# Performance work log

Measured on AMD Instinct MI355X. Metric: run time of the kernel, lower is better.

The kernel has to match this reference:

```python
import jax, jax.numpy as jnp
import numpy as np
import math

HEAD_DIM = 128
LAMBDA_INIT = 0.8


def setup_inputs() -> dict:
    key = jax.random.key(0)
    ks = jax.random.split(key, 5)
    B, H, HKV, S, D = 1, 16, 4, 2048, HEAD_DIM
    return {
        "q1": jax.random.normal(ks[0], (B, H, S, D), jnp.float32),
        "k1": jax.random.normal(ks[1], (B, HKV, S, D), jnp.float32),
        "v": jax.random.normal(ks[2], (B, HKV, S, D), jnp.float32),
        "q2": jax.random.normal(ks[3], (B, H, S, D), jnp.float32),
        "k2": jax.random.normal(ks[4], (B, HKV, S, D), jnp.float32),
        "lambda_log": jnp.full((1,), math.log(LAMBDA_INIT), jnp.float32),
    }


def _sdpa(q, k, v, scale):
    # q: [b,h,s,d]; k,v already repeated to h heads
    s = jnp.einsum("bhqd,bhkd->bhqk", q, k) * scale
    w = jax.nn.softmax(s, axis=-1)
    return jnp.einsum("bhqk,bhkd->bhqd", w, v)


def reference(q1, k1, v, q2, k2, lambda_log):
    H = q1.shape[1]
    HKV = k1.shape[1]
    rep = H // HKV
    if rep > 1:
        k1 = jnp.repeat(k1, rep, axis=1)
        k2 = jnp.repeat(k2, rep, axis=1)
        v = jnp.repeat(v, rep, axis=1)
    scale = q1.shape[-1] ** -0.5
    attn1 = _sdpa(q1, k1, v, scale)
    attn2 = _sdpa(q2, k2, v, scale)
    lam = jnp.exp(lambda_log).astype(q1.dtype)  # shape (1,), broadcasts
    return attn1 - lam * attn2
```

## Files before the change

### kernel.cpp

```cpp
#include <hip/hip_runtime.h>
#include <hip/hip_bf16.h>
#include <stdint.h>

#define D 128
#define SEQ 2048
#define NH 16
#define KVB 64
#define NTILE 32
#define BLOCK_Q 128

typedef float f32x4  __attribute__((ext_vector_type(4)));
typedef float f32x16 __attribute__((ext_vector_type(16)));
typedef short bf16x8 __attribute__((ext_vector_type(8)));

__device__ __forceinline__ unsigned cvtpk(float lo, float hi){
    unsigned r;
    asm("v_cvt_pk_bf16_f32 %0, %1, %2" : "=v"(r) : "v"(lo), "v"(hi));
    return r;
}

__global__ __launch_bounds__(256) void prep(const float* __restrict__ k1,
                                            const float* __restrict__ k2,
                                            const float* __restrict__ v,
                                            char* __restrict__ ws)
{
    int cid = blockIdx.x * 256 + threadIdx.x;
    if (cid < 262144){
        const float* src = (cid & 131072) ? k2 : k1;
        int r    = cid & 131071;
        int grow = r >> 4;
        int c16  = r & 15;
        const float* p = src + (size_t)grow * D + ((c16 ^ (grow & 7)) << 3);
        f32x4 a = *(const f32x4*)p;
        f32x4 b = *(const f32x4*)(p + 4);
        uint4 w;
        w.x = cvtpk(a[0], a[1]); w.y = cvtpk(a[2], a[3]);
        w.z = cvtpk(b[0], b[1]); w.w = cvtpk(b[2], b[3]);
        *(uint4*)(ws + (size_t)cid * 16) = w;
    } else {
        int r   = cid - 262144;
        int d   = (r >> 3) & 127;
        int c16 = r & 7;
        int gk  = ((r >> 10) << 6) + ((c16 ^ (d & 7)) << 3);
        const float* p = v + (size_t)gk * D + d;
        uint4 w;
        w.x = cvtpk(p[0*D], p[1*D]);
        w.y = cvtpk(p[2*D], p[3*D]);
        w.z = cvtpk(p[4*D], p[5*D]);
        w.w = cvtpk(p[6*D], p[7*D]);
        *(uint4*)(ws + 4194304 + (size_t)r * 16) = w;
    }
}

struct Buf { char k1[16384]; char k2[16384]; char vt[16384]; };
union LdsU { Buf buf[2]; float oepi[BLOCK_Q * D]; };

__global__ __launch_bounds__(512, 2)
void diffattn(const float* __restrict__ q1, const float* __restrict__ q2,
              const float* __restrict__ ll, const char* __restrict__ ws,
              float* __restrict__ out)
{
    __shared__ LdsU lds;
    const int tid  = threadIdx.x;
    const int lane = tid & 63;
    const int wid  = tid >> 6;
    const int atn  = wid >> 2;
    const int wq   = wid & 3;
    const int g    = lane >> 5;
    const int ql   = lane & 31;

    const int bid  = blockIdx.x;
    const int sbid = (bid & 7) * 32 + (bid >> 3);
    const int qb   = sbid & 15;
    const int h    = sbid >> 4;
    const int kvh  = h >> 2;

    auto stage = [&](int b, int t){
        const char* base = ws + ((size_t)(kvh * NTILE + t) << 14) + (lane << 4);
        char* lb = (char*)&lds.buf[b];
        #pragma unroll
        for (int j = 0; j < 6; ++j){
            int ci  = wid * 6 + j;
            int mat = ci >> 4, sub = ci & 15;
            __builtin_amdgcn_global_load_lds(
                (const __attribute__((address_space(1))) void*)(base + (size_t)mat * 2097152 + (sub << 10)),
                (__attribute__((address_space(3))) void*)(lb + mat * 16384 + (sub << 10)),
                16, 0, 0);
        }
    };
    stage(0, 0);

    const float* Qbase = (atn ? q2 : q1)
        + ((size_t)h * SEQ + (size_t)qb * BLOCK_Q + wq * 32 + ql) * D;
    const float qsc = 0.08838834764831845f * 1.4426950408889634f;
    bf16x8 qf[8];
    #pragma unroll
    for (int dc = 0; dc < 8; ++dc){
        const float* p = Qbase + dc * 16 + g * 8;
        f32x4 a = *(const f32x4*)(p);
        f32x4 b = *(const f32x4*)(p + 4);
        union { bf16x8 v; unsigned u[4]; } u;
        u.u[0] = cvtpk(a[0] * qsc, a[1] * qsc);
        u.u[1] = cvtpk(a[2] * qsc, a[3] * qsc);
        u.u[2] = cvtpk(b[0] * qsc, b[1] * qsc);
        u.u[3] = cvtpk(b[2] * qsc, b[3] * qsc);
        qf[dc] = u.v;
    }

    f32x16 ot[4];
    #pragma unroll
    for (int i = 0; i < 4; ++i){
        #pragma unroll
        for (int e = 0; e < 16; ++e) ot[i][e] = 0.f;
    }
    float mrun = -1e30f, lrun = 0.f;

    __syncthreads();

    for (int t = 0; t < NTILE; ++t){
        const int cur = t & 1;
        if (t + 1 < NTILE) stage(cur ^ 1, t + 1);

        const char* kt = atn ? lds.buf[cur].k2 : lds.buf[cur].k1;
        const char* vt = lds.buf[cur].vt;

        f32x16 st[2];
        __builtin_amdgcn_s_setprio(1);
        #pragma unroll
        for (int kb = 0; kb < 2; ++kb){
            f32x16 acc;
            #pragma unroll
            for (int e = 0; e < 16; ++e) acc[e] = 0.f;
            const int krow = kb * 32 + ql;
            const int kswz = (krow & 7) << 4;
            #pragma unroll
            for (int dc = 0; dc < 8; ++dc){
                bf16x8 kf = *(const bf16x8*)(kt + ((krow * 256 + dc * 32 + g * 16) ^ kswz));
                acc = __builtin_amdgcn_mfma_f32_32x32x16_bf16(kf, qf[dc], acc, 0, 0, 0);
            }
            st[kb] = acc;
        }
        __builtin_amdgcn_s_setprio(0);

        float tmax = -1e30f;
        #pragma unroll
        for (int kb = 0; kb < 2; ++kb){
            #pragma unroll
            for (int e = 0; e < 16; ++e) tmax = fmaxf(tmax, st[kb][e]);
        }
        tmax = fmaxf(tmax, __shfl_xor(tmax, 32));
        if (!__all(tmax <= mrun + 8.f)){
            float mnew = fmaxf(mrun, tmax);
            float corr = exp2f(mrun - mnew);
            lrun *= corr;
            #pragma unroll
            for (int i = 0; i < 4; ++i) ot[i] = ot[i] * corr;
            mrun = mnew;
        }
        float p[2][16];
        float ps = 0.f;
        #pragma unroll
        for (int kb = 0; kb < 2; ++kb){
            #pragma unroll
            for (int e = 0; e < 16; ++e){
                float pe = exp2f(st[kb][e] - mrun);
                p[kb][e] = pe; ps += pe;
            }
        }
        ps += __shfl_xor(ps, 32);
        lrun += ps;

        unsigned W[2][4][2];
        #pragma unroll
        for (int kb = 0; kb < 2; ++kb){
            #pragma unroll
            for (int hh = 0; hh < 4; ++hh){
                #pragma unroll
                for (int jj = 0; jj < 2; ++jj)
                    W[kb][hh][jj] = cvtpk(p[kb][4*hh + 2*jj], p[kb][4*hh + 2*jj + 1]);
            }
        }
        bf16x8 pb[4];
        #pragma unroll
        for (int kc = 0; kc < 4; ++kc){
            const int kb = kc >> 1, b0 = 2 * (kc & 1);
            union { bf16x8 v; unsigned u[4]; } pu;
            #pragma unroll
            for (int j = 0; j < 4; ++j){
                const int gsrc = j >> 1, jj = j & 1;
                unsigned wlo = W[kb][b0][jj];
                unsigned whi = W[kb][b0 + 1][jj];
                unsigned loc = g ? whi : wlo;
                unsigned oth = g ? wlo : whi;
                unsigned rem = (unsigned)__shfl_xor((int)oth, 32);
                pu.u[j] = (gsrc == g) ? loc : rem;
            }
            pb[kc] = pu.v;
        }

        __builtin_amdgcn_s_setprio(1);
        #pragma unroll
        for (int db = 0; db < 4; ++db){
            const int drow = db * 32 + ql;
            const int vswz = (drow & 7) << 4;
            #pragma unroll
            for (int kc = 0; kc < 4; ++kc){
                bf16x8 vf = *(const bf16x8*)(vt + ((drow * 128 + kc * 32 + g * 16) ^ vswz));
                ot[db] = __builtin_amdgcn_mfma_f32_32x32x16_bf16(vf, pb[kc], ot[db], 0, 0, 0);
            }
        }
        __builtin_amdgcn_s_setprio(0);
        __syncthreads();
    }

    const float lam = expf(ll[0]);
    const float inv = 1.f / lrun;
    const int rowl = wq * 32 + ql;
    const int eswz = (rowl & 7) << 2;

    if (atn == 1){
        const float s = -lam * inv;
        #pragma unroll
        for (int db = 0; db < 4; ++db){
            #pragma unroll
            for (int e = 0; e < 16; ++e){
                int d = db * 32 + (e & 3) + 8 * (e >> 2) + 4 * g;
                lds.oepi[rowl * 128 + (d ^ eswz)] = ot[db][e] * s;
            }
        }
    }
    __syncthreads();
    if (atn == 0){
        #pragma unroll
        for (int db = 0; db < 4; ++db){
            #pragma unroll
            for (int e = 0; e < 16; ++e){
                int d = db * 32 + (e & 3) + 8 * (e >> 2) + 4 * g;
                int idx = rowl * 128 + (d ^ eswz);
                lds.oepi[idx] = ot[db][e] * inv + lds.oepi[idx];
            }
        }
    }
    __syncthreads();

    const size_t obase = ((size_t)h * SEQ + (size_t)qb * BLOCK_Q) * D;
    const int row = tid >> 2;
    const int q4  = tid & 3;
    const int sw  = (row & 7) << 2;
    #pragma unroll
    for (int j = 0; j < 8; ++j){
        int c = q4 * 32 + j * 4;
        f32x4 val = *(const f32x4*)&lds.oepi[row * 128 + (c ^ sw)];
        *(f32x4*)(out + obase + (size_t)row * D + c) = val;
    }
}

extern "C" void kernel_launch(void* const* d_in, const int* in_sizes, int n_in,
                              void* d_out, int out_size, void* d_ws, size_t ws_size,
                              hipStream_t stream)
{
    (void)in_sizes; (void)n_in; (void)out_size; (void)ws_size;
    const float* q1 = (const float*)d_in[0];
    const float* k1 = (const float*)d_in[1];
    const float* v  = (const float*)d_in[2];
    const float* q2 = (const float*)d_in[3];
    const float* k2 = (const float*)d_in[4];
    const float* ll = (const float*)d_in[5];
    prep<<<1536, 256, 0, stream>>>(k1, k2, v, (char*)d_ws);
    diffattn<<<256, 512, 0, stream>>>(q1, q2, ll, (const char*)d_ws, (float*)d_out);
}
```

Before: 183.7 us.

## Give each wave two query sub-tiles and transpose V through LDS in prep

The attention kernel drops to 256 threads, with each wave handling 64 query rows as two 32-row sub-tiles. Each K and V fragment read from LDS now feeds two MFMAs, which halves LDS fragment traffic per FLOP, at the cost of double the accumulator registers and one block per CU. The prep kernel's V transpose now reads coalesced rows into a padded LDS buffer and writes the transposed bf16 tiles from there, replacing the old strided column gathers. This also shrinks prep's grid.

```diff
diff --git a/kernel.cpp b/kernel.cpp
--- a/kernel.cpp
+++ b/kernel.cpp
@@ -8,6 +8,7 @@
 #define KVB 64
 #define NTILE 32
 #define BLOCK_Q 128
+#define QT 64
 
 typedef float f32x4  __attribute__((ext_vector_type(4)));
 typedef float f32x16 __attribute__((ext_vector_type(16)));
@@ -19,43 +20,69 @@
     return r;
 }
 
+#define VSTRIDE 130
 __global__ __launch_bounds__(256) void prep(const float* __restrict__ k1,
                                             const float* __restrict__ k2,
                                             const float* __restrict__ v,
                                             char* __restrict__ ws)
 {
-    int cid = blockIdx.x * 256 + threadIdx.x;
-    if (cid < 262144){
+    __shared__ unsigned short vlds[64 * VSTRIDE];
+    const int b = blockIdx.x;
+    if (b < 1024){
+        int cid = b * 256 + threadIdx.x;
         const float* src = (cid & 131072) ? k2 : k1;
         int r    = cid & 131071;
         int grow = r >> 4;
         int c16  = r & 15;
         const float* p = src + (size_t)grow * D + ((c16 ^ (grow & 7)) << 3);
         f32x4 a = *(const f32x4*)p;
-        f32x4 b = *(const f32x4*)(p + 4);
+        f32x4 c = *(const f32x4*)(p + 4);
         uint4 w;
         w.x = cvtpk(a[0], a[1]); w.y = cvtpk(a[2], a[3]);
-        w.z = cvtpk(b[0], b[1]); w.w = cvtpk(b[2], b[3]);
+        w.z = cvtpk(c[0], c[1]); w.w = cvtpk(c[2], c[3]);
         *(uint4*)(ws + (size_t)cid * 16) = w;
     } else {
-        int r   = cid - 262144;
-        int d   = (r >> 3) & 127;
-        int c16 = r & 7;
-        int gk  = ((r >> 10) << 6) + ((c16 ^ (d & 7)) << 3);
-        const float* p = v + (size_t)gk * D + d;
-        uint4 w;
-        w.x = cvtpk(p[0*D], p[1*D]);
-        w.y = cvtpk(p[2*D], p[3*D]);
-        w.z = cvtpk(p[4*D], p[5*D]);
-        w.w = cvtpk(p[6*D], p[7*D]);
-        *(uint4*)(ws + 4194304 + (size_t)r * 16) = w;
+        const int vt  = b - 1024;
+        const int tid = threadIdx.x;
+        const size_t gkb = (size_t)vt * 64;
+        const int key = tid >> 2, cg = tid & 3;
+        const float* vp = v + (gkb + key) * D + cg * 32;
+        #pragma unroll
+        for (int i = 0; i < 8; ++i){
+            f32x4 x = *(const f32x4*)(vp + i * 4);
+            unsigned lo = cvtpk(x[0], x[1]);
+            unsigned hi = cvtpk(x[2], x[3]);
+            unsigned* dst = (unsigned*)&vlds[key * VSTRIDE + cg * 32 + i * 4];
+            dst[0] = lo; dst[1] = hi;
+        }
+        __syncthreads();
+        char* outb = ws + 4194304 + ((size_t)vt << 14);
+        #pragma unroll
+        for (int i = 0; i < 4; ++i){
+            int c   = tid + 256 * i;
+            int d   = c >> 3;
+            int c16 = c & 7;
+            int m   = (c16 ^ (d & 7)) << 3;
+            unsigned v0 = vlds[(m + 0) * VSTRIDE + d];
+            unsigned v1 = vlds[(m + 1) * VSTRIDE + d];
+            unsigned v2 = vlds[(m + 2) * VSTRIDE + d];
+            unsigned v3 = vlds[(m + 3) * VSTRIDE + d];
+            unsigned v4 = vlds[(m + 4) * VSTRIDE + d];
+            unsigned v5 = vlds[(m + 5) * VSTRIDE + d];
+            unsigned v6 = vlds[(m + 6) * VSTRIDE + d];
+            unsigned v7 = vlds[(m + 7) * VSTRIDE + d];
+            uint4 w;
+            w.x = v0 | (v1 << 16); w.y = v2 | (v3 << 16);
+            w.z = v4 | (v5 << 16); w.w = v6 | (v7 << 16);
+            *(uint4*)(outb + (size_t)c * 16) = w;
+        }
     }
 }
 
 struct Buf { char k1[16384]; char k2[16384]; char vt[16384]; };
 union LdsU { Buf buf[2]; float oepi[BLOCK_Q * D]; };
 
-__global__ __launch_bounds__(512, 2)
+__global__ __launch_bounds__(256, 1)
 void diffattn(const float* __restrict__ q1, const float* __restrict__ q2,
               const float* __restrict__ ll, const char* __restrict__ ws,
               float* __restrict__ out)
@@ -64,8 +91,8 @@
     const int tid  = threadIdx.x;
     const int lane = tid & 63;
     const int wid  = tid >> 6;
-    const int atn  = wid >> 2;
-    const int wq   = wid & 3;
+    const int atn  = wid >> 1;
+    const int wq   = wid & 1;
     const int g    = lane >> 5;
     const int ql   = lane & 31;
 
@@ -75,12 +102,12 @@
     const int h    = sbid >> 4;
     const int kvh  = h >> 2;
 
-    auto stage = [&](int b, int t){
+    auto stage = [&](int bsel, int t){
         const char* base = ws + ((size_t)(kvh * NTILE + t) << 14) + (lane << 4);
-        char* lb = (char*)&lds.buf[b];
-        #pragma unroll
-        for (int j = 0; j < 6; ++j){
-            int ci  = wid * 6 + j;
+        char* lb = (char*)&lds.buf[bsel];
+        #pragma unroll
+        for (int j = 0; j < 12; ++j){
+            int ci  = wid * 12 + j;
             int mat = ci >> 4, sub = ci & 15;
             __builtin_amdgcn_global_load_lds(
                 (const __attribute__((address_space(1))) void*)(base + (size_t)mat * 2097152 + (sub << 10)),
@@ -90,30 +117,34 @@
     };
     stage(0, 0);
 
-    const float* Qbase = (atn ? q2 : q1)
-        + ((size_t)h * SEQ + (size_t)qb * BLOCK_Q + wq * 32 + ql) * D;
     const float qsc = 0.08838834764831845f * 1.4426950408889634f;
-    bf16x8 qf[8];
+    bf16x8 qf[2][8];
     #pragma unroll
-    for (int dc = 0; dc < 8; ++dc){
-        const float* p = Qbase + dc * 16 + g * 8;
-        f32x4 a = *(const f32x4*)(p);
-        f32x4 b = *(const f32x4*)(p + 4);
-        union { bf16x8 v; unsigned u[4]; } u;
-        u.u[0] = cvtpk(a[0] * qsc, a[1] * qsc);
-        u.u[1] = cvtpk(a[2] * qsc, a[3] * qsc);
-        u.u[2] = cvtpk(b[0] * qsc, b[1] * qsc);
-        u.u[3] = cvtpk(b[2] * qsc, b[3] * qsc);
-        qf[dc] = u.v;
-    }
-
-    f32x16 ot[4];
+    for (int qs = 0; qs < 2; ++qs){
+        const float* Qbase = (atn ? q2 : q1)
+            + ((size_t)h * SEQ + (size_t)qb * BLOCK_Q + wq * QT + qs * 32 + ql) * D;
+        #pragma unroll
+        for (int dc = 0; dc < 8; ++dc){
+            const float* p = Qbase + dc * 16 + g * 8;
+            f32x4 a = *(const f32x4*)(p);
+            f32x4 c = *(const f32x4*)(p + 4);
+            union { bf16x8 v; unsigned u[4]; } u;
+            u.u[0] = cvtpk(a[0] * qsc, a[1] * qsc);
+            u.u[1] = cvtpk(a[2] * qsc, a[3] * qsc);
+            u.u[2] = cvtpk(c[0] * qsc, c[1] * qsc);
+            u.u[3] = cvtpk(c[2] * qsc, c[3] * qsc);
+            qf[qs][dc] = u.v;
+        }
+    }
+
+    f32x16 ot[2][4];
     #pragma unroll
-    for (int i = 0; i < 4; ++i){
-        #pragma unroll
-        for (int e = 0; e < 16; ++e) ot[i][e] = 0.f;
-    }
-    float mrun = -1e30f, lrun = 0.f;
+    for (int qs = 0; qs < 2; ++qs)
+        #pragma unroll
+        for (int i = 0; i < 4; ++i)
+            #pragma unroll
+            for (int e = 0; e < 16; ++e) ot[qs][i][e] = 0.f;
+    float mrun[2] = {-1e30f, -1e30f}, lrun[2] = {0.f, 0.f};
 
     __syncthreads();
 
@@ -124,78 +155,78 @@
         const char* kt = atn ? lds.buf[cur].k2 : lds.buf[cur].k1;
         const char* vt = lds.buf[cur].vt;
 
-        f32x16 st[2];
+        f32x16 st[2][2];
         __builtin_amdgcn_s_setprio(1);
         #pragma unroll
         for (int kb = 0; kb < 2; ++kb){
-            f32x16 acc;
-            #pragma unroll
-            for (int e = 0; e < 16; ++e) acc[e] = 0.f;
+            #pragma unroll
+            for (int qs = 0; qs < 2; ++qs)
+                #pragma unroll
+                for (int e = 0; e < 16; ++e) st[qs][kb][e] = 0.f;
             const int krow = kb * 32 + ql;
             const int kswz = (krow & 7) << 4;
             #pragma unroll
             for (int dc = 0; dc < 8; ++dc){
                 bf16x8 kf = *(const bf16x8*)(kt + ((krow * 256 + dc * 32 + g * 16) ^ kswz));
-                acc = __builtin_amdgcn_mfma_f32_32x32x16_bf16(kf, qf[dc], acc, 0, 0, 0);
+                st[0][kb] = __builtin_amdgcn_mfma_f32_32x32x16_bf16(kf, qf[0][dc], st[0][kb], 0, 0, 0);
+                st[1][kb] = __builtin_amdgcn_mfma_f32_32x32x16_bf16(kf, qf[1][dc], st[1][kb], 0, 0, 0);
             }
-            st[kb] = acc;
         }
         __builtin_amdgcn_s_setprio(0);
 
-        float tmax = -1e30f;
-        #pragma unroll
-        for (int kb = 0; kb < 2; ++kb){
-            #pragma unroll
-            for (int e = 0; e < 16; ++e) tmax = fmaxf(tmax, st[kb][e]);
-        }
-        tmax = fmaxf(tmax, __shfl_xor(tmax, 32));
-        if (!__all(tmax <= mrun + 8.f)){
-            float mnew = fmaxf(mrun, tmax);
-            float corr = exp2f(mrun - mnew);
-            lrun *= corr;
-            #pragma unroll
-            for (int i = 0; i < 4; ++i) ot[i] = ot[i] * corr;
-            mrun = mnew;
-        }
-        float p[2][16];
-        float ps = 0.f;
-        #pragma unroll
-        for (int kb = 0; kb < 2; ++kb){
-            #pragma unroll
-            for (int e = 0; e < 16; ++e){
-                float pe = exp2f(st[kb][e] - mrun);
-                p[kb][e] = pe; ps += pe;
+        bf16x8 pb[2][4];
+        #pragma unroll
+        for (int qs = 0; qs < 2; ++qs){
+            float tmax = -1e30f;
+            #pragma unroll
+            for (int kb = 0; kb < 2; ++kb)
+                #pragma unroll
+                for (int e = 0; e < 16; ++e) tmax = fmaxf(tmax, st[qs][kb][e]);
+            tmax = fmaxf(tmax, __shfl_xor(tmax, 32));
+            if (!__all(tmax <= mrun[qs] + 8.f)){
+                float mnew = fmaxf(mrun[qs], tmax);
+                float corr = exp2f(mrun[qs] - mnew);
+                lrun[qs] *= corr;
+                #pragma unroll
+                for (int i = 0; i < 4; ++i) ot[qs][i] = ot[qs][i] * corr;
+                mrun[qs] = mnew;
             }
-        }
-        ps += __shfl_xor(ps, 32);
-        lrun += ps;
-
-        unsigned W[2][4][2];
-        #pragma unroll
-        for (int kb = 0; kb < 2; ++kb){
-            #pragma unroll
-            for (int hh = 0; hh < 4; ++hh){
-                #pragma unroll
-                for (int jj = 0; jj < 2; ++jj)
-                    W[kb][hh][jj] = cvtpk(p[kb][4*hh + 2*jj], p[kb][4*hh + 2*jj + 1]);
+            float p[2][16];
+            float ps = 0.f;
+            #pragma unroll
+            for (int kb = 0; kb < 2; ++kb)
+                #pragma unroll
+                for (int e = 0; e < 16; ++e){
+                    float pe = exp2f(st[qs][kb][e] - mrun[qs]);
+                    p[kb][e] = pe; ps += pe;
+                }
+            ps += __shfl_xor(ps, 32);
+            lrun[qs] += ps;
+
+            unsigned W[2][4][2];
+            #pragma unroll
+            for (int kb = 0; kb < 2; ++kb)
+                #pragma unroll
+                for (int hh = 0; hh < 4; ++hh)
+                    #pragma unroll
+                    for (int jj = 0; jj < 2; ++jj)
+                        W[kb][hh][jj] = cvtpk(p[kb][4*hh + 2*jj], p[kb][4*hh + 2*jj + 1]);
+            #pragma unroll
+            for (int kc = 0; kc < 4; ++kc){
+                const int kb = kc >> 1, b0 = 2 * (kc & 1);
+                union { bf16x8 v; unsigned u[4]; } pu;
+                #pragma unroll
+                for (int j = 0; j < 4; ++j){
+                    const int gsrc = j >> 1, jj = j & 1;
+                    unsigned wlo = W[kb][b0][jj];
+                    unsigned whi = W[kb][b0 + 1][jj];
+                    unsigned loc = g ? whi : wlo;
+                    unsigned oth = g ? wlo : whi;
+                    unsigned rem = (unsigned)__shfl_xor((int)oth, 32);
+                    pu.u[j] = (gsrc == g) ? loc : rem;
+                }
+                pb[qs][kc] = pu.v;
             }
-        }
-        bf16x8 pb[4];
-        #pragma unroll
-        for (int kc = 0; kc < 4; ++kc){
-            const int kb = kc >> 1, b0 = 2 * (kc & 1);
-            union { bf16x8 v; unsigned u[4]; } pu;
-            #pragma unroll
-            for (int j = 0; j < 4; ++j){
-                const int gsrc = j >> 1, jj = j & 1;
-                unsigned wlo = W[kb][b0][jj];
-                unsigned whi = W[kb][b0 + 1][jj];
-                unsigned loc = g ? whi : wlo;
-                unsigned oth = g ? wlo : whi;
-                unsigned rem = (unsigned)__shfl_xor((int)oth, 32);
-                pu.u[j] = (gsrc == g) ? loc : rem;
-            }
-            pb[kc] = pu.v;
         }
 
         __builtin_amdgcn_s_setprio(1);
@@ -206,7 +237,8 @@
             #pragma unroll
             for (int kc = 0; kc < 4; ++kc){
                 bf16x8 vf = *(const bf16x8*)(vt + ((drow * 128 + kc * 32 + g * 16) ^ vswz));
-                ot[db] = __builtin_amdgcn_mfma_f32_32x32x16_bf16(vf, pb[kc], ot[db], 0, 0, 0);
+                ot[0][db] = __builtin_amdgcn_mfma_f32_32x32x16_bf16(vf, pb[0][kc], ot[0][db], 0, 0, 0);
+                ot[1][db] = __builtin_amdgcn_mfma_f32_32x32x16_bf16(vf, pb[1][kc], ot[1][db], 0, 0, 0);
             }
         }
         __builtin_amdgcn_s_setprio(0);
@@ -214,43 +246,58 @@
     }
 
     const float lam = expf(ll[0]);
-    const float inv = 1.f / lrun;
-    const int rowl = wq * 32 + ql;
-    const int eswz = (rowl & 7) << 2;
 
     if (atn == 1){
-        const float s = -lam * inv;
-        #pragma unroll
-        for (int db = 0; db < 4; ++db){
-            #pragma unroll
-            for (int e = 0; e < 16; ++e){
-                int d = db * 32 + (e & 3) + 8 * (e >> 2) + 4 * g;
-                lds.oepi[rowl * 128 + (d ^ eswz)] = ot[db][e] * s;
-            }
+        #pragma unroll
+        for (int qs = 0; qs < 2; ++qs){
+            const float s = -lam / lrun[qs];
+            const int rowl = wq * QT + qs * 32 + ql;
+            const int eswz = (rowl & 7) << 2;
+            #pragma unroll
+            for (int db = 0; db < 4; ++db)
+                #pragma unroll
+                for (int e = 0; e < 16; ++e){
+                    int d = db * 32 + (e & 3) + 8 * (e >> 2) + 4 * g;
+                    lds.oepi[rowl * 128 + (d ^ eswz)] = ot[qs][db][e] * s;
+                }
         }
     }
     __syncthreads();
     if (atn == 0){
         #pragma unroll
-        for (int db = 0; db < 4; ++db){
-            #pragma unroll
-            for (int e = 0; e < 16; ++e){
-                int d = db * 32 + (e & 3) + 8 * (e >> 2) + 4 * g;
-                int idx = rowl * 128 + (d ^ eswz);
-                lds.oepi[idx] = ot[db][e] * inv + lds.oepi[idx];
-            }
+        for (int qs = 0; qs < 2; ++qs){
+            const float inv = 1.f / lrun[qs];
+            const int rowl = wq * QT + qs * 32 + ql;
+            const int eswz = (rowl & 7) << 2;
+            #pragma unroll
+            for (int db = 0; db < 4; ++db)
+                #pragma unroll
+                for (int e = 0; e < 16; ++e){
+                    int d = db * 32 + (e & 3) + 8 * (e >> 2) + 4 * g;
+                    int idx = rowl * 128 + (d ^ eswz);
+                    lds.oepi[idx] = ot[qs][db][e] * inv + lds.oepi[idx];
+                }
         }
     }
     __syncthreads();
 
     const size_t obase = ((size_t)h * SEQ + (size_t)qb * BLOCK_Q) * D;
-    const int row = tid >> 2;
-    const int q4  = tid & 3;
+    const int row = tid >> 1;
+    const int ch  = (tid & 1) * 64;
     const int sw  = (row & 7) << 2;
     #pragma unroll
-    for (int j = 0; j < 8; ++j){
-        int c = q4 * 32 + j * 4;
+    for (int j = 0; j < 4; ++j){
+        int c = ch + j * 16;
         f32x4 val = *(const f32x4*)&lds.oepi[row * 128 + (c ^ sw)];
+        *(f32x4*)(out + obase + (size_t)row * D + c) = val;
+        c += 4;
+        val = *(const f32x4*)&lds.oepi[row * 128 + (c ^ sw)];
+        *(f32x4*)(out + obase + (size_t)row * D + c) = val;
+        c += 4;
+        val = *(const f32x4*)&lds.oepi[row * 128 + (c ^ sw)];
+        *(f32x4*)(out + obase + (size_t)row * D + c) = val;
+        c += 4;
+        val = *(const f32x4*)&lds.oepi[row * 128 + (c ^ sw)];
         *(f32x4*)(out + obase + (size_t)row * D + c) = val;
     }
 }
@@ -266,6 +313,6 @@
     const float* q2 = (const float*)d_in[3];
     const float* k2 = (const float*)d_in[4];
     const float* ll = (const float*)d_in[5];
-    prep<<<1536, 256, 0, stream>>>(k1, k2, v, (char*)d_ws);
-    diffattn<<<256, 512, 0, stream>>>(q1, q2, ll, (const char*)d_ws, (float*)d_out);
+    prep<<<1152, 256, 0, stream>>>(k1, k2, v, (char*)d_ws);
+    diffattn<<<256, 256, 0, stream>>>(q1, q2, ll, (const char*)d_ws, (float*)d_out);
 }
```

New measurement: 226.1 us. +23.1%, slower.

## Halve query and KV tiles, fold max offset into MFMA init, transpose V via LDS

Applied to the files above, without the earlier changes.

The attention kernel now uses 64-row query blocks and 32-key tiles, launched as 512 blocks of 256 threads instead of 256 blocks of 512. This halves LDS per buffer and gives more blocks to spread across CUs. The running max is pre-subtracted by initializing the QK accumulator with -m, which removes a subtract per score. The prep kernel now transposes V through shared memory with coalesced fp32 reads, replacing the old strided global reads. The trade-off is twice as many KV-tile iterations and barriers, and K/V tiles are reloaded once per smaller query block.

```diff
diff --git a/kernel.cpp b/kernel.cpp
--- a/kernel.cpp
+++ b/kernel.cpp
@@ -5,9 +5,9 @@
 #define D 128
 #define SEQ 2048
 #define NH 16
-#define KVB 64
-#define NTILE 32
-#define BLOCK_Q 128
+#define KVB 32
+#define NTILE 64
+#define BLOCK_Q 64
 
 typedef float f32x4  __attribute__((ext_vector_type(4)));
 typedef float f32x16 __attribute__((ext_vector_type(16)));
@@ -19,43 +19,71 @@
     return r;
 }
 
+#define VSTRIDE 130
 __global__ __launch_bounds__(256) void prep(const float* __restrict__ k1,
                                             const float* __restrict__ k2,
                                             const float* __restrict__ v,
                                             char* __restrict__ ws)
 {
-    int cid = blockIdx.x * 256 + threadIdx.x;
-    if (cid < 262144){
+    __shared__ unsigned short vlds[64 * VSTRIDE];
+    const int b = blockIdx.x;
+    if (b < 1024){
+        int cid = b * 256 + threadIdx.x;
         const float* src = (cid & 131072) ? k2 : k1;
         int r    = cid & 131071;
         int grow = r >> 4;
         int c16  = r & 15;
         const float* p = src + (size_t)grow * D + ((c16 ^ (grow & 7)) << 3);
         f32x4 a = *(const f32x4*)p;
-        f32x4 b = *(const f32x4*)(p + 4);
+        f32x4 c = *(const f32x4*)(p + 4);
         uint4 w;
         w.x = cvtpk(a[0], a[1]); w.y = cvtpk(a[2], a[3]);
-        w.z = cvtpk(b[0], b[1]); w.w = cvtpk(b[2], b[3]);
+        w.z = cvtpk(c[0], c[1]); w.w = cvtpk(c[2], c[3]);
         *(uint4*)(ws + (size_t)cid * 16) = w;
     } else {
-        int r   = cid - 262144;
-        int d   = (r >> 3) & 127;
-        int c16 = r & 7;
-        int gk  = ((r >> 10) << 6) + ((c16 ^ (d & 7)) << 3);
-        const float* p = v + (size_t)gk * D + d;
-        uint4 w;
-        w.x = cvtpk(p[0*D], p[1*D]);
-        w.y = cvtpk(p[2*D], p[3*D]);
-        w.z = cvtpk(p[4*D], p[5*D]);
-        w.w = cvtpk(p[6*D], p[7*D]);
-        *(uint4*)(ws + 4194304 + (size_t)r * 16) = w;
-    }
-}
-
-struct Buf { char k1[16384]; char k2[16384]; char vt[16384]; };
+        const int vt  = b - 1024;
+        const int tid = threadIdx.x;
+        const int key = tid >> 2, cg = tid & 3;
+        const float* vp = v + (size_t)(vt * 64 + key) * D + cg * 32;
+        #pragma unroll
+        for (int i = 0; i < 8; ++i){
+            f32x4 x = *(const f32x4*)(vp + i * 4);
+            unsigned lo = cvtpk(x[0], x[1]);
+            unsigned hi = cvtpk(x[2], x[3]);
+            unsigned* dst = (unsigned*)&vlds[key * VSTRIDE + cg * 32 + i * 4];
+            dst[0] = lo; dst[1] = hi;
+        }
+        __syncthreads();
+        #pragma unroll
+        for (int tt = 0; tt < 2; ++tt){
+            char* outb = ws + 4194304 + (((size_t)vt * 2 + tt) << 13);
+            #pragma unroll
+            for (int i = 0; i < 2; ++i){
+                int c = tid + 256 * i;
+                int d = c >> 2;
+                int s = c & 3;
+                int m = tt * 32 + ((s ^ (d & 3)) << 3);
+                unsigned v0 = vlds[(m + 0) * VSTRIDE + d];
+                unsigned v1 = vlds[(m + 1) * VSTRIDE + d];
+                unsigned v2 = vlds[(m + 2) * VSTRIDE + d];
+                unsigned v3 = vlds[(m + 3) * VSTRIDE + d];
+                unsigned v4 = vlds[(m + 4) * VSTRIDE + d];
+                unsigned v5 = vlds[(m + 5) * VSTRIDE + d];
+                unsigned v6 = vlds[(m + 6) * VSTRIDE + d];
+                unsigned v7 = vlds[(m + 7) * VSTRIDE + d];
+                uint4 w;
+                w.x = v0 | (v1 << 16); w.y = v2 | (v3 << 16);
+                w.z = v4 | (v5 << 16); w.w = v6 | (v7 << 16);
+                *(uint4*)(outb + (size_t)c * 16) = w;
+            }
+        }
+    }
+}
+
+struct Buf { char k1[8192]; char k2[8192]; char vt[8192]; };
 union LdsU { Buf buf[2]; float oepi[BLOCK_Q * D]; };
 
-__global__ __launch_bounds__(512, 2)
+__global__ __launch_bounds__(256, 2)
 void diffattn(const float* __restrict__ q1, const float* __restrict__ q2,
               const float* __restrict__ ll, const char* __restrict__ ws,
               float* __restrict__ out)
@@ -64,27 +92,30 @@
     const int tid  = threadIdx.x;
     const int lane = tid & 63;
     const int wid  = tid >> 6;
-    const int atn  = wid >> 2;
-    const int wq   = wid & 3;
+    const int atn  = wid >> 1;
+    const int wq   = wid & 1;
     const int g    = lane >> 5;
     const int ql   = lane & 31;
 
     const int bid  = blockIdx.x;
-    const int sbid = (bid & 7) * 32 + (bid >> 3);
-    const int qb   = sbid & 15;
-    const int h    = sbid >> 4;
+    const int sbid = (bid & 7) * 64 + (bid >> 3);
+    const int qb   = sbid & 31;
+    const int h    = sbid >> 5;
     const int kvh  = h >> 2;
 
-    auto stage = [&](int b, int t){
-        const char* base = ws + ((size_t)(kvh * NTILE + t) << 14) + (lane << 4);
-        char* lb = (char*)&lds.buf[b];
+    auto stage = [&](int bsel, int t){
+        const char* b1 = ws + ((size_t)(kvh * 2048 + t * KVB) << 8);
+        const char* b2 = b1 + 2097152;
+        const char* bv = ws + 4194304 + ((size_t)(kvh * NTILE + t) << 13);
+        char* lb = (char*)&lds.buf[bsel];
         #pragma unroll
         for (int j = 0; j < 6; ++j){
             int ci  = wid * 6 + j;
-            int mat = ci >> 4, sub = ci & 15;
+            int mat = ci >> 3, sub = ci & 7;
+            const char* gb = (mat == 0) ? b1 : ((mat == 1) ? b2 : bv);
             __builtin_amdgcn_global_load_lds(
-                (const __attribute__((address_space(1))) void*)(base + (size_t)mat * 2097152 + (sub << 10)),
-                (__attribute__((address_space(3))) void*)(lb + mat * 16384 + (sub << 10)),
+                (const __attribute__((address_space(1))) void*)(gb + (sub << 10) + (lane << 4)),
+                (__attribute__((address_space(3))) void*)(lb + mat * 8192 + (sub << 10)),
                 16, 0, 0);
         }
     };
@@ -98,22 +129,21 @@
     for (int dc = 0; dc < 8; ++dc){
         const float* p = Qbase + dc * 16 + g * 8;
         f32x4 a = *(const f32x4*)(p);
-        f32x4 b = *(const f32x4*)(p + 4);
+        f32x4 c = *(const f32x4*)(p + 4);
         union { bf16x8 v; unsigned u[4]; } u;
         u.u[0] = cvtpk(a[0] * qsc, a[1] * qsc);
         u.u[1] = cvtpk(a[2] * qsc, a[3] * qsc);
-        u.u[2] = cvtpk(b[0] * qsc, b[1] * qsc);
-        u.u[3] = cvtpk(b[2] * qsc, b[3] * qsc);
+        u.u[2] = cvtpk(c[0] * qsc, c[1] * qsc);
+        u.u[3] = cvtpk(c[2] * qsc, c[3] * qsc);
         qf[dc] = u.v;
     }
 
     f32x16 ot[4];
     #pragma unroll
-    for (int i = 0; i < 4; ++i){
+    for (int i = 0; i < 4; ++i)
         #pragma unroll
         for (int e = 0; e < 16; ++e) ot[i][e] = 0.f;
-    }
-    float mrun = -1e30f, lrun = 0.f;
+    float mrun = 0.f, lrun = 0.f;
 
     __syncthreads();
 
@@ -122,79 +152,65 @@
         if (t + 1 < NTILE) stage(cur ^ 1, t + 1);
 
         const char* kt = atn ? lds.buf[cur].k2 : lds.buf[cur].k1;
-        const char* vt = lds.buf[cur].vt;
-
-        f32x16 st[2];
+        const char* vtp = lds.buf[cur].vt;
+
+        f32x16 st;
+        const float negm = -mrun;
+        #pragma unroll
+        for (int e = 0; e < 16; ++e) st[e] = negm;
+        const int kswz = (ql & 7) << 4;
         __builtin_amdgcn_s_setprio(1);
         #pragma unroll
-        for (int kb = 0; kb < 2; ++kb){
-            f32x16 acc;
-            #pragma unroll
-            for (int e = 0; e < 16; ++e) acc[e] = 0.f;
-            const int krow = kb * 32 + ql;
-            const int kswz = (krow & 7) << 4;
-            #pragma unroll
-            for (int dc = 0; dc < 8; ++dc){
-                bf16x8 kf = *(const bf16x8*)(kt + ((krow * 256 + dc * 32 + g * 16) ^ kswz));
-                acc = __builtin_amdgcn_mfma_f32_32x32x16_bf16(kf, qf[dc], acc, 0, 0, 0);
-            }
-            st[kb] = acc;
+        for (int dc = 0; dc < 8; ++dc){
+            bf16x8 kf = *(const bf16x8*)(kt + ((ql * 256 + dc * 32 + g * 16) ^ kswz));
+            st = __builtin_amdgcn_mfma_f32_32x32x16_bf16(kf, qf[dc], st, 0, 0, 0);
         }
         __builtin_amdgcn_s_setprio(0);
 
-        float tmax = -1e30f;
-        #pragma unroll
-        for (int kb = 0; kb < 2; ++kb){
-            #pragma unroll
-            for (int e = 0; e < 16; ++e) tmax = fmaxf(tmax, st[kb][e]);
-        }
+        float tmax = st[0];
+        #pragma unroll
+        for (int e = 1; e < 16; ++e) tmax = fmaxf(tmax, st[e]);
         tmax = fmaxf(tmax, __shfl_xor(tmax, 32));
-        if (!__all(tmax <= mrun + 8.f)){
-            float mnew = fmaxf(mrun, tmax);
-            float corr = exp2f(mrun - mnew);
+        if (!__all(tmax <= 8.f)){
+            float tpos = fmaxf(tmax, 0.f);
+            float corr = exp2f(-tpos);
             lrun *= corr;
             #pragma unroll
             for (int i = 0; i < 4; ++i) ot[i] = ot[i] * corr;
-            mrun = mnew;
-        }
-        float p[2][16];
+            mrun += tpos;
+            #pragma unroll
+            for (int e = 0; e < 16; ++e) st[e] -= tpos;
+        }
+        float p[16];
         float ps = 0.f;
         #pragma unroll
-        for (int kb = 0; kb < 2; ++kb){
-            #pragma unroll
-            for (int e = 0; e < 16; ++e){
-                float pe = exp2f(st[kb][e] - mrun);
-                p[kb][e] = pe; ps += pe;
-            }
+        for (int e = 0; e < 16; ++e){
+            float pe = exp2f(st[e]);
+            p[e] = pe; ps += pe;
         }
         ps += __shfl_xor(ps, 32);
         lrun += ps;
 
-        unsigned W[2][4][2];
-        #pragma unroll
-        for (int kb = 0; kb < 2; ++kb){
-            #pragma unroll
-            for (int hh = 0; hh < 4; ++hh){
-                #pragma unroll
-                for (int jj = 0; jj < 2; ++jj)
-                    W[kb][hh][jj] = cvtpk(p[kb][4*hh + 2*jj], p[kb][4*hh + 2*jj + 1]);
-            }
-        }
-        bf16x8 pb[4];
-        #pragma unroll
-        for (int kc = 0; kc < 4; ++kc){
-            const int kb = kc >> 1, b0 = 2 * (kc & 1);
+        unsigned W[4][2];
+        #pragma unroll
+        for (int hh = 0; hh < 4; ++hh)
+            #pragma unroll
+            for (int jj = 0; jj < 2; ++jj)
+                W[hh][jj] = cvtpk(p[4*hh + 2*jj], p[4*hh + 2*jj + 1]);
+        bf16x8 pb[2];
+        #pragma unroll
+        for (int kc = 0; kc < 2; ++kc){
+            unsigned a0 = W[2*kc][0],   a1 = W[2*kc][1];
+            unsigned b0 = W[2*kc+1][0], b1 = W[2*kc+1][1];
+            unsigned loc0 = g ? b0 : a0, loc1 = g ? b1 : a1;
+            unsigned snd0 = g ? a0 : b0, snd1 = g ? a1 : b1;
+            unsigned rem0 = (unsigned)__shfl_xor((int)snd0, 32);
+            unsigned rem1 = (unsigned)__shfl_xor((int)snd1, 32);
             union { bf16x8 v; unsigned u[4]; } pu;
-            #pragma unroll
-            for (int j = 0; j < 4; ++j){
-                const int gsrc = j >> 1, jj = j & 1;
-                unsigned wlo = W[kb][b0][jj];
-                unsigned whi = W[kb][b0 + 1][jj];
-                unsigned loc = g ? whi : wlo;
-                unsigned oth = g ? wlo : whi;
-                unsigned rem = (unsigned)__shfl_xor((int)oth, 32);
-                pu.u[j] = (gsrc == g) ? loc : rem;
-            }
+            pu.u[0] = g ? rem0 : loc0;
+            pu.u[1] = g ? rem1 : loc1;
+            pu.u[2] = g ? loc0 : rem0;
+            pu.u[3] = g ? loc1 : rem1;
             pb[kc] = pu.v;
         }
 
@@ -202,10 +218,10 @@
         #pragma unroll
         for (int db = 0; db < 4; ++db){
             const int drow = db * 32 + ql;
-            const int vswz = (drow & 7) << 4;
-            #pragma unroll
-            for (int kc = 0; kc < 4; ++kc){
-                bf16x8 vf = *(const bf16x8*)(vt + ((drow * 128 + kc * 32 + g * 16) ^ vswz));
+            #pragma unroll
+            for (int kc = 0; kc < 2; ++kc){
+                int s = (kc * 2 + g) ^ (drow & 3);
+                bf16x8 vf = *(const bf16x8*)(vtp + drow * 64 + s * 16);
                 ot[db] = __builtin_amdgcn_mfma_f32_32x32x16_bf16(vf, pb[kc], ot[db], 0, 0, 0);
             }
         }
@@ -214,42 +230,40 @@
     }
 
     const float lam = expf(ll[0]);
-    const float inv = 1.f / lrun;
     const int rowl = wq * 32 + ql;
     const int eswz = (rowl & 7) << 2;
 
     if (atn == 1){
-        const float s = -lam * inv;
-        #pragma unroll
-        for (int db = 0; db < 4; ++db){
+        const float s = -lam / lrun;
+        #pragma unroll
+        for (int db = 0; db < 4; ++db)
             #pragma unroll
             for (int e = 0; e < 16; ++e){
                 int d = db * 32 + (e & 3) + 8 * (e >> 2) + 4 * g;
                 lds.oepi[rowl * 128 + (d ^ eswz)] = ot[db][e] * s;
             }
-        }
     }
     __syncthreads();
     if (atn == 0){
-        #pragma unroll
-        for (int db = 0; db < 4; ++db){
+        const float inv = 1.f / lrun;
+        #pragma unroll
+        for (int db = 0; db < 4; ++db)
             #pragma unroll
             for (int e = 0; e < 16; ++e){
                 int d = db * 32 + (e & 3) + 8 * (e >> 2) + 4 * g;
                 int idx = rowl * 128 + (d ^ eswz);
                 lds.oepi[idx] = ot[db][e] * inv + lds.oepi[idx];
             }
-        }
     }
     __syncthreads();
 
     const size_t obase = ((size_t)h * SEQ + (size_t)qb * BLOCK_Q) * D;
     const int row = tid >> 2;
-    const int q4  = tid & 3;
+    const int qc  = tid & 3;
     const int sw  = (row & 7) << 2;
     #pragma unroll
     for (int j = 0; j < 8; ++j){
-        int c = q4 * 32 + j * 4;
+        int c = qc * 32 + j * 4;
         f32x4 val = *(const f32x4*)&lds.oepi[row * 128 + (c ^ sw)];
         *(f32x4*)(out + obase + (size_t)row * D + c) = val;
     }
@@ -266,6 +280,6 @@
     const float* q2 = (const float*)d_in[3];
     const float* k2 = (const float*)d_in[4];
     const float* ll = (const float*)d_in[5];
-    prep<<<1536, 256, 0, stream>>>(k1, k2, v, (char*)d_ws);
-    diffattn<<<256, 512, 0, stream>>>(q1, q2, ll, (const char*)d_ws, (float*)d_out);
-}
+    prep<<<1152, 256, 0, stream>>>(k1, k2, v, (char*)d_ws);
+    diffattn<<<512, 256, 0, stream>>>(q1, q2, ll, (const char*)d_ws, (float*)d_out);
+}
```

After: 198.4 us. 8.0% more time.
